# Kernel optimization log

Measured on AMD Instinct MI355X. Metric: run time of the kernel, lower is better.

Reference implementation:

```python
import jax, jax.numpy as jnp
import numpy as np

N_CLASSES = 256
N_AUDIO_CHANS = 1
N_CHANS = 128
N_RES = 128
N_SKIP = 256
N_END = 256
KERNEL = 2
N_LAYERS = 10
N_STACKS = 3
DILATIONS = [2 ** i for _ in range(N_STACKS) for i in range(N_LAYERS)]
L = len(DILATIONS)
DN = ('NCW', 'OIW', 'NCW')


def setup_inputs() -> dict:
    key = jax.random.key(0)
    ks = jax.random.split(key, 16)
    s = 0.05  # small init keeps 30-layer residual stack numerically tame
    inp = {
        'x': jax.random.normal(ks[0], (4, N_AUDIO_CHANS, 16384), jnp.float32),
        'w_shift': jax.random.normal(ks[1], (N_CHANS, N_AUDIO_CHANS, KERNEL), jnp.float32) * s,
        'b_shift': jnp.zeros((N_CHANS,), jnp.float32),
        'conv_w': jax.random.normal(ks[2], (L, 2 * N_RES, N_CHANS, KERNEL), jnp.float32) * s,
        'conv_b': jnp.zeros((L, 2 * N_RES), jnp.float32),
        'res_w': jax.random.normal(ks[3], (L, N_CHANS, N_RES), jnp.float32) * s,
        'res_b': jnp.zeros((L, N_CHANS), jnp.float32),
        'skip_w': jax.random.normal(ks[4], (L, N_SKIP, N_RES), jnp.float32) * s,
        'skip_b': jnp.zeros((L, N_SKIP), jnp.float32),
        'a_w': jax.random.normal(ks[5], (N_END, N_SKIP), jnp.float32) * s,
        'a_b': jnp.zeros((N_END,), jnp.float32),
        'b_w': jax.random.normal(ks[6], (N_CLASSES * N_AUDIO_CHANS, N_END), jnp.float32) * s,
        'b_b': jnp.zeros((N_CLASSES * N_AUDIO_CHANS,), jnp.float32),
    }
    return inp


def _causal_conv(x, w, b, dilation):
    # left-pad by (k-1)*dilation so outputs depend only on past/present
    pad = (w.shape[-1] - 1) * dilation
    xp = jnp.pad(x, ((0, 0), (0, 0), (pad, 0)))
    y = jax.lax.conv_general_dilated(xp, w, window_strides=(1,), padding='VALID',
                                     rhs_dilation=(dilation,), dimension_numbers=DN)
    return y + b[None, :, None]


def reference(x, w_shift, b_shift, conv_w, conv_b, res_w, res_b,
              skip_w, skip_b, a_w, a_b, b_w, b_b):
    N, C, W = x.shape
    # shifted conv: shift input right by one (prepend 0, drop last), then causal conv
    xs = jnp.pad(x, ((0, 0), (0, 0), (1, 0)))[:, :, :-1]
    h = _causal_conv(xs, w_shift, b_shift, 1)  # (N, n_chans, W)

    skips = jnp.zeros((N, N_SKIP, W), h.dtype)
    for l in range(L):
        g = _causal_conv(h, conv_w[l], conv_b[l], DILATIONS[l])  # (N, 2*res, W)
        a, b_gate = jnp.split(g, 2, axis=1)
        gated = a * jax.nn.sigmoid(b_gate)                        # GLU, (N, res, W)
        h = jnp.einsum('or,nrw->now', res_w[l], gated) + res_b[l][None, :, None] + h
        skips = skips + jnp.einsum('or,nrw->now', skip_w[l], gated) + skip_b[l][None, :, None]

    z = jax.nn.relu(skips)
    z = jax.nn.relu(jnp.einsum('os,nsw->now', a_w, z) + a_b[None, :, None])
    logits = jnp.einsum('oe,new->now', b_w, z) + b_b[None, :, None]
    return logits.reshape(N, N_CLASSES, N_AUDIO_CHANS, W)
```

## Files before the change

kernel.cpp:

```cpp
#include <hip/hip_runtime.h>
#include <math.h>


#define NB 4
#define WLEN 16384
#define C 128
#define S 256
#define NLAYERS 30
#define TT 64
#define NTB (WLEN / TT)
#define XROW 264
#define GROW 136

typedef _Float16 half8 __attribute__((ext_vector_type(8)));
typedef _Float16 half4 __attribute__((ext_vector_type(4)));
typedef float floatx4 __attribute__((ext_vector_type(4)));

__device__ __forceinline__ float sigmoidf_(float v) {
    return 1.0f / (1.0f + __expf(-v));
}

__global__ void prep_kernel(const float* __restrict__ conv_w,
                            const float* __restrict__ res_w,
                            const float* __restrict__ skip_w,
                            const float* __restrict__ a_w,
                            const float* __restrict__ b_w,
                            const float* __restrict__ conv_b,
                            const float* __restrict__ skip_b,
                            _Float16* __restrict__ cw,
                            _Float16* __restrict__ rsw,
                            _Float16* __restrict__ skw,
                            _Float16* __restrict__ aw,
                            _Float16* __restrict__ bw,
                            float* __restrict__ cbp,
                            float* __restrict__ ssum) {
    const int ncw = NLAYERS * 256 * 256;
    const int nrs = NLAYERS * 128 * 128;
    const int nsk = NLAYERS * 256 * 128;
    const int nab = 256 * 256;
    const int ncb = NLAYERS * 256;
    const int total = ncw + nrs + nsk + nab + nab + ncb + 256;
    for (int idx = blockIdx.x * blockDim.x + threadIdx.x; idx < total;
         idx += gridDim.x * blockDim.x) {
        int i = idx;
        if (i < ncw) {
            int j = i & 7, lane = (i >> 3) & 63, rest = i >> 9;
            int ks = rest & 7; rest >>= 3;
            int mt = rest & 15; int l = rest >> 4;
            int mp = mt * 16 + (lane & 15);
            int orow = (mp >> 1) + (mp & 1) * 128;
            int k = ks * 32 + (lane >> 4) * 8 + j;
            int tap = k >> 7, c = k & 127;
            cw[i] = (_Float16)conv_w[(((size_t)l * 256 + orow) * 128 + c) * 2 + tap];
        } else if (i < ncw + nrs) {
            i -= ncw;
            int j = i & 7, lane = (i >> 3) & 63, rest = i >> 9;
            int ks = rest & 3; rest >>= 2;
            int mt = rest & 7; int l = rest >> 3;
            int m = mt * 16 + (lane & 15);
            int k = ks * 32 + (lane >> 4) * 8 + j;
            rsw[i] = (_Float16)res_w[((size_t)l * 128 + m) * 128 + k];
        } else if (i < ncw + nrs + nsk) {
            i -= ncw + nrs;
            int j = i & 7, lane = (i >> 3) & 63, rest = i >> 9;
            int ks = rest & 3; rest >>= 2;
            int mt = rest & 15; int l = rest >> 4;
            int m = mt * 16 + (lane & 15);
            int k = ks * 32 + (lane >> 4) * 8 + j;
            skw[i] = (_Float16)skip_w[((size_t)l * 256 + m) * 128 + k];
        } else if (i < ncw + nrs + nsk + nab) {
            i -= ncw + nrs + nsk;
            int j = i & 7, lane = (i >> 3) & 63, rest = i >> 9;
            int ks = rest & 7; int mt = rest >> 3;
            aw[i] = (_Float16)a_w[(mt * 16 + (lane & 15)) * 256 + ks * 32 + (lane >> 4) * 8 + j];
        } else if (i < ncw + nrs + nsk + 2 * nab) {
            i -= ncw + nrs + nsk + nab;
            int j = i & 7, lane = (i >> 3) & 63, rest = i >> 9;
            int ks = rest & 7; int mt = rest >> 3;
            bw[i] = (_Float16)b_w[(mt * 16 + (lane & 15)) * 256 + ks * 32 + (lane >> 4) * 8 + j];
        } else if (i < ncw + nrs + nsk + 2 * nab + ncb) {
            i -= ncw + nrs + nsk + 2 * nab;
            int mp = i & 255; int l = i >> 8;
            cbp[i] = conv_b[l * 256 + (mp >> 1) + (mp & 1) * 128];
        } else {
            i -= ncw + nrs + nsk + 2 * nab + ncb;
            float s = 0.f;
            for (int l = 0; l < NLAYERS; ++l) s += skip_b[l * 256 + i];
            ssum[i] = s;
        }
    }
}

__global__ void front_kernel(const float* __restrict__ x,
                             const float* __restrict__ w_shift,
                             const float* __restrict__ b_shift,
                             _Float16* __restrict__ h) {
    const int n = blockIdx.y;
    const int t = blockIdx.x * 256 + threadIdx.x;
    float x1 = (t >= 1) ? x[n * WLEN + t - 1] : 0.0f;
    float x2 = (t >= 2) ? x[n * WLEN + t - 2] : 0.0f;
    _Float16* hq = h + ((size_t)n * WLEN + t) * 128;
    #pragma unroll
    for (int c0 = 0; c0 < 128; c0 += 8) {
        half8 v;
        #pragma unroll
        for (int j = 0; j < 8; ++j) {
            int c = c0 + j;
            v[j] = (_Float16)fmaf(w_shift[2 * c], x2,
                                  fmaf(w_shift[2 * c + 1], x1, b_shift[c]));
        }
        *(half8*)&hq[c0] = v;
    }
}

template <bool FIRST>
__global__ __launch_bounds__(512, 8) void layer_kernel(
    const _Float16* __restrict__ h_in, _Float16* __restrict__ h_out,
    _Float16* __restrict__ chunk,
    const _Float16* __restrict__ cw, const float* __restrict__ cb,
    const _Float16* __restrict__ rsw, const float* __restrict__ rb,
    const _Float16* __restrict__ skw, const float* __restrict__ ssum, int d) {
    __shared__ _Float16 SMEM[2 * TT * GROW];
    _Float16* X0 = SMEM;
    _Float16* X1 = SMEM + TT * GROW;
    _Float16* G  = X0;
    const int n = blockIdx.y, tb = blockIdx.x, t0 = tb * TT;
    const int tid = threadIdx.x;
    const int wave = __builtin_amdgcn_readfirstlane(tid >> 6);
    const int lane = tid & 63, q = lane >> 4, ml = lane & 15;

    const _Float16* hn = h_in + (size_t)n * WLEN * 128;
    #pragma unroll
    for (int it = 0; it < 4; ++it) {
        int idx = it * 512 + tid;
        int seg = idx & 15;
        int rowc = (idx >> 4) & 63;
        int tap = idx >> 10;
        int src_t = t0 + rowc - (tap ? 0 : d);
        half8 v = (half8)(_Float16)0.0f;
        if (src_t >= 0)
            v = *(const half8*)&hn[(size_t)src_t * 128 + seg * 8];
        _Float16* Xb = tap ? X1 : X0;
        *(half8*)&Xb[rowc * GROW + seg * 8] = v;
    }
    __syncthreads();

    floatx4 acc[2][4];
    #pragma unroll
    for (int mt = 0; mt < 2; ++mt)
        #pragma unroll
        for (int r = 0; r < 4; ++r) {
            float bias = cb[32 * wave + mt * 16 + q * 4 + r];
            #pragma unroll
            for (int nt = 0; nt < 4; ++nt) acc[mt][nt][r] = bias;
        }
    #pragma unroll
    for (int hp = 0; hp < 2; ++hp) {
        const _Float16* Xb = hp ? X1 : X0;
        for (int ks = 0; ks < 4; ++ks) {
            half8 a[2];
            #pragma unroll
            for (int mt = 0; mt < 2; ++mt)
                a[mt] = *(const half8*)&cw[((((2 * wave + mt) * 8) + hp * 4 + ks) * 64 + lane) * 8];
            #pragma unroll
            for (int nt = 0; nt < 4; ++nt) {
                half8 b = *(const half8*)&Xb[(nt * 16 + ml) * GROW + ks * 32 + q * 8];
                #pragma unroll
                for (int mt = 0; mt < 2; ++mt)
                    acc[mt][nt] = __builtin_amdgcn_mfma_f32_16x16x32_f16(a[mt], b, acc[mt][nt], 0, 0, 0);
            }
        }
    }
    __syncthreads();

    #pragma unroll
    for (int mt = 0; mt < 2; ++mt)
        #pragma unroll
        for (int nt = 0; nt < 4; ++nt) {
            float g0 = acc[mt][nt][0] * sigmoidf_(acc[mt][nt][1]);
            float g1 = acc[mt][nt][2] * sigmoidf_(acc[mt][nt][3]);
            _Float16 p[2] = {(_Float16)g0, (_Float16)g1};
            *(uint32_t*)&G[(nt * 16 + ml) * GROW + 16 * wave + mt * 8 + 2 * q] = *(uint32_t*)p;
        }
    __syncthreads();

    {
        floatx4 sacc[2][4];
        #pragma unroll
        for (int mt = 0; mt < 2; ++mt)
            #pragma unroll
            for (int r = 0; r < 4; ++r) {
                float bias = FIRST ? ssum[32 * wave + mt * 16 + q * 4 + r] : 0.0f;
                #pragma unroll
                for (int nt = 0; nt < 4; ++nt) sacc[mt][nt][r] = bias;
            }
        #pragma unroll
        for (int ks = 0; ks < 4; ++ks) {
            half8 a[2];
            #pragma unroll
            for (int mt = 0; mt < 2; ++mt)
                a[mt] = *(const half8*)&skw[((((2 * wave + mt) * 4) + ks) * 64 + lane) * 8];
            #pragma unroll
            for (int nt = 0; nt < 4; ++nt) {
                half8 b = *(const half8*)&G[(nt * 16 + ml) * GROW + ks * 32 + q * 8];
                #pragma unroll
                for (int mt = 0; mt < 2; ++mt)
                    sacc[mt][nt] = __builtin_amdgcn_mfma_f32_16x16x32_f16(a[mt], b, sacc[mt][nt], 0, 0, 0);
            }
        }
        _Float16* cp = chunk + ((size_t)n * NTB + tb) * 16384;
        #pragma unroll
        for (int mt = 0; mt < 2; ++mt)
            #pragma unroll
            for (int nt = 0; nt < 4; ++nt) {
                size_t o = (size_t)((((wave * 2 + mt) * 4) + nt) * 64 + lane) * 4;
                if (FIRST) {
                    half4 v;
                    #pragma unroll
                    for (int r = 0; r < 4; ++r) v[r] = (_Float16)sacc[mt][nt][r];
                    *(half4*)&cp[o] = v;
                } else {
                    half4 v = *(const half4*)&cp[o];
                    half4 w;
                    #pragma unroll
                    for (int r = 0; r < 4; ++r)
                        w[r] = (_Float16)(sacc[mt][nt][r] + (float)v[r]);
                    *(half4*)&cp[o] = w;
                }
            }
    }

    {
        floatx4 racc[4];
        #pragma unroll
        for (int r = 0; r < 4; ++r) {
            float bias = rb[16 * wave + q * 4 + r];
            #pragma unroll
            for (int nt = 0; nt < 4; ++nt) racc[nt][r] = bias;
        }
        #pragma unroll
        for (int ks = 0; ks < 4; ++ks) {
            half8 a = *(const half8*)&rsw[(((wave * 4) + ks) * 64 + lane) * 8];
            #pragma unroll
            for (int nt = 0; nt < 4; ++nt) {
                half8 b = *(const half8*)&G[(nt * 16 + ml) * GROW + ks * 32 + q * 8];
                racc[nt] = __builtin_amdgcn_mfma_f32_16x16x32_f16(a, b, racc[nt], 0, 0, 0);
            }
        }
        _Float16* ho = h_out + (size_t)n * WLEN * 128;
        #pragma unroll
        for (int nt = 0; nt < 4; ++nt) {
            int tt = nt * 16 + ml;
            int c = 16 * wave + q * 4;
            half4 hv = *(const half4*)&X1[tt * GROW + c];
            half4 o;
            #pragma unroll
            for (int r = 0; r < 4; ++r)
                o[r] = (_Float16)(racc[nt][r] + (float)hv[r]);
            *(half4*)&ho[(size_t)(t0 + tt) * 128 + c] = o;
        }
    }
}

__global__ __launch_bounds__(512, 8) void head_kernel(
    float* __restrict__ out, const _Float16* __restrict__ chunk,
    const _Float16* __restrict__ aw, const float* __restrict__ ab,
    const _Float16* __restrict__ bw, const float* __restrict__ bb) {
    __shared__ _Float16 X[TT * XROW];
    const int n = blockIdx.y, tb = blockIdx.x, t0 = tb * TT;
    const int tid = threadIdx.x;
    const int wave = __builtin_amdgcn_readfirstlane(tid >> 6);
    const int lane = tid & 63, q = lane >> 4, ml = lane & 15;

    {
        const _Float16* cp = chunk + ((size_t)n * NTB + tb) * 16384;
        #pragma unroll
        for (int mt = 0; mt < 2; ++mt)
            #pragma unroll
            for (int nt = 0; nt < 4; ++nt) {
                size_t o = (size_t)((((wave * 2 + mt) * 4) + nt) * 64 + lane) * 4;
                half4 v = *(const half4*)&cp[o];
                half4 z;
                #pragma unroll
                for (int r = 0; r < 4; ++r)
                    z[r] = (_Float16)fmaxf((float)v[r], 0.0f);
                *(half4*)&X[(nt * 16 + ml) * XROW + 32 * wave + mt * 16 + q * 4] = z;
            }
    }
    __syncthreads();

    floatx4 acc[2][4];
    #pragma unroll
    for (int mt = 0; mt < 2; ++mt)
        #pragma unroll
        for (int r = 0; r < 4; ++r) {
            float bias = ab[32 * wave + mt * 16 + q * 4 + r];
            #pragma unroll
            for (int nt = 0; nt < 4; ++nt) acc[mt][nt][r] = bias;
        }
    for (int ks = 0; ks < 8; ++ks) {
        half8 a[2];
        #pragma unroll
        for (int mt = 0; mt < 2; ++mt)
            a[mt] = *(const half8*)&aw[((((2 * wave + mt) * 8) + ks) * 64 + lane) * 8];
        #pragma unroll
        for (int nt = 0; nt < 4; ++nt) {
            half8 b = *(const half8*)&X[(nt * 16 + ml) * XROW + ks * 32 + q * 8];
            #pragma unroll
            for (int mt = 0; mt < 2; ++mt)
                acc[mt][nt] = __builtin_amdgcn_mfma_f32_16x16x32_f16(a[mt], b, acc[mt][nt], 0, 0, 0);
        }
    }
    __syncthreads();
    #pragma unroll
    for (int mt = 0; mt < 2; ++mt)
        #pragma unroll
        for (int nt = 0; nt < 4; ++nt) {
            half4 z;
            #pragma unroll
            for (int r = 0; r < 4; ++r)
                z[r] = (_Float16)fmaxf(acc[mt][nt][r], 0.0f);
            *(half4*)&X[(nt * 16 + ml) * XROW + 32 * wave + mt * 16 + q * 4] = z;
        }
    __syncthreads();

    #pragma unroll
    for (int mt = 0; mt < 2; ++mt)
        #pragma unroll
        for (int r = 0; r < 4; ++r) {
            float bias = bb[32 * wave + mt * 16 + q * 4 + r];
            #pragma unroll
            for (int nt = 0; nt < 4; ++nt) acc[mt][nt][r] = bias;
        }
    for (int ks = 0; ks < 8; ++ks) {
        half8 a[2];
        #pragma unroll
        for (int mt = 0; mt < 2; ++mt)
            a[mt] = *(const half8*)&bw[((((2 * wave + mt) * 8) + ks) * 64 + lane) * 8];
        #pragma unroll
        for (int nt = 0; nt < 4; ++nt) {
            half8 b = *(const half8*)&X[(nt * 16 + ml) * XROW + ks * 32 + q * 8];
            #pragma unroll
            for (int mt = 0; mt < 2; ++mt)
                acc[mt][nt] = __builtin_amdgcn_mfma_f32_16x16x32_f16(a[mt], b, acc[mt][nt], 0, 0, 0);
        }
    }
    float* on = out + (size_t)n * S * WLEN;
    #pragma unroll
    for (int mt = 0; mt < 2; ++mt)
        #pragma unroll
        for (int nt = 0; nt < 4; ++nt)
            #pragma unroll
            for (int r = 0; r < 4; ++r) {
                int o = 32 * wave + mt * 16 + q * 4 + r;
                int tt = t0 + nt * 16 + ml;
                on[(size_t)o * WLEN + tt] = acc[mt][nt][r];
            }
}

extern "C" void kernel_launch(void* const* d_in, const int* in_sizes, int n_in,
                              void* d_out, int out_size, void* d_ws, size_t ws_size,
                              hipStream_t stream) {
    (void)in_sizes; (void)n_in; (void)out_size; (void)ws_size;
    const float* x       = (const float*)d_in[0];
    const float* w_shift = (const float*)d_in[1];
    const float* b_shift = (const float*)d_in[2];
    const float* conv_w  = (const float*)d_in[3];
    const float* conv_b  = (const float*)d_in[4];
    const float* res_w   = (const float*)d_in[5];
    const float* res_b   = (const float*)d_in[6];
    const float* skip_w  = (const float*)d_in[7];
    const float* skip_b  = (const float*)d_in[8];
    const float* a_w     = (const float*)d_in[9];
    const float* a_b     = (const float*)d_in[10];
    const float* b_w     = (const float*)d_in[11];
    const float* b_b     = (const float*)d_in[12];
    float* out = (float*)d_out;

    char* ws = (char*)d_ws;
    size_t off = 0;
    _Float16* hA    = (_Float16*)(ws + off); off += (size_t)NB * WLEN * 128 * 2;
    _Float16* hB    = (_Float16*)(ws + off); off += (size_t)NB * WLEN * 128 * 2;
    _Float16* chunk = (_Float16*)(ws + off); off += (size_t)NB * NTB * 16384 * 2;
    _Float16* cw  = (_Float16*)(ws + off); off += (size_t)NLAYERS * 256 * 256 * 2;
    _Float16* rsw = (_Float16*)(ws + off); off += (size_t)NLAYERS * 128 * 128 * 2;
    _Float16* skw = (_Float16*)(ws + off); off += (size_t)NLAYERS * 256 * 128 * 2;
    _Float16* aw  = (_Float16*)(ws + off); off += 256 * 256 * 2;
    _Float16* bw  = (_Float16*)(ws + off); off += 256 * 256 * 2;
    float* cbp  = (float*)(ws + off); off += (size_t)NLAYERS * 256 * 4;
    float* ssum = (float*)(ws + off); off += 256 * 4;

    prep_kernel<<<512, 256, 0, stream>>>(conv_w, res_w, skip_w, a_w, b_w,
                                         conv_b, skip_b,
                                         cw, rsw, skw, aw, bw, cbp, ssum);
    front_kernel<<<dim3(WLEN / 256, NB), 256, 0, stream>>>(x, w_shift, b_shift, hA);

    const dim3 grid(NTB, NB);
    _Float16* hin = hA;
    _Float16* hout = hB;
    for (int l = 0; l < NLAYERS; ++l) {
        int dil = 1 << (l % 10);
        const _Float16* cwp = cw + (size_t)l * 65536;
        const _Float16* rsp = rsw + (size_t)l * 16384;
        const _Float16* skp = skw + (size_t)l * 32768;
        if (l == 0)
            layer_kernel<true><<<grid, 512, 0, stream>>>(
                hin, hout, chunk, cwp, cbp + l * 256,
                rsp, res_b + l * 128, skp, ssum, dil);
        else
            layer_kernel<false><<<grid, 512, 0, stream>>>(
                hin, hout, chunk, cwp, cbp + l * 256,
                rsp, res_b + l * 128, skp, ssum, dil);
        _Float16* tmp = hin; hin = hout; hout = tmp;
    }

    head_kernel<<<grid, 512, 0, stream>>>(out, chunk, aw, a_b, bw, b_b);
}
```

Measured before the change: 1.100 ms.

## Fuse first six dilated layers of each stack into one halo-tiled kernel

Measured after the change: 1.099 ms. No clear change (-0.1%).

```diff
diff --git a/kernel.cpp b/kernel.cpp
--- a/kernel.cpp
+++ b/kernel.cpp
@@ -11,6 +11,7 @@
 #define NTB (WLEN / TT)
 #define XROW 264
 #define GROW 136
+#define HW 128
 
 typedef _Float16 half8 __attribute__((ext_vector_type(8)));
 typedef _Float16 half4 __attribute__((ext_vector_type(4)));
@@ -114,12 +115,189 @@
 }
 
 template <bool FIRST>
+__global__ __launch_bounds__(512, 4) void stack_kernel(
+    const _Float16* __restrict__ h_in, _Float16* __restrict__ h_out,
+    _Float16* __restrict__ chunk,
+    const _Float16* __restrict__ cw0, const float* __restrict__ cb0,
+    const _Float16* __restrict__ rsw0, const float* __restrict__ rb0,
+    const _Float16* __restrict__ skw0, const float* __restrict__ ssum) {
+    __shared__ _Float16 SMEM[2 * HW * GROW];
+    _Float16* H = SMEM;
+    _Float16* G = SMEM + HW * GROW;
+    const int n = blockIdx.y, tb = blockIdx.x, t0 = tb * TT;
+    const int tid = threadIdx.x;
+    const int wave = __builtin_amdgcn_readfirstlane(tid >> 6);
+    const int lane = tid & 63, q = lane >> 4, ml = lane & 15;
+
+    floatx4 sacc[2][4];
+    if (FIRST) {
+        #pragma unroll
+        for (int mt = 0; mt < 2; ++mt)
+            #pragma unroll
+            for (int r = 0; r < 4; ++r) {
+                float bias = ssum[32 * wave + mt * 16 + q * 4 + r];
+                #pragma unroll
+                for (int nt = 0; nt < 4; ++nt) sacc[mt][nt][r] = bias;
+            }
+    } else {
+        const _Float16* cp = chunk + ((size_t)n * NTB + tb) * 16384;
+        #pragma unroll
+        for (int mt = 0; mt < 2; ++mt)
+            #pragma unroll
+            for (int nt = 0; nt < 4; ++nt) {
+                size_t o = (size_t)((((wave * 2 + mt) * 4) + nt) * 64 + lane) * 4;
+                half4 v = *(const half4*)&cp[o];
+                #pragma unroll
+                for (int r = 0; r < 4; ++r) sacc[mt][nt][r] = (float)v[r];
+            }
+    }
+
+    const _Float16* hn = h_in + (size_t)n * WLEN * 128;
+    #pragma unroll
+    for (int it = 0; it < 4; ++it) {
+        int idx = it * 512 + tid;
+        int seg = idx & 15;
+        int w = idx >> 4;
+        int src_t = t0 - 64 + w;
+        half8 v = (half8)(_Float16)0.0f;
+        if (src_t >= 0)
+            v = *(const half8*)&hn[(size_t)src_t * 128 + seg * 8];
+        *(half8*)&H[w * GROW + seg * 8] = v;
+    }
+    __syncthreads();
+
+    const _Float16* cw  = cw0;
+    const float*    cb  = cb0;
+    const _Float16* rsw = rsw0;
+    const float*    rb  = rb0;
+    const _Float16* skw = skw0;
+
+    #pragma clang loop unroll(disable)
+    for (int j = 0; j < 6; ++j) {
+        const int d = 1 << j;
+
+        #pragma unroll
+        for (int np = 0; np < 2; ++np) {
+            floatx4 acc[2][4];
+            #pragma unroll
+            for (int mt = 0; mt < 2; ++mt)
+                #pragma unroll
+                for (int r = 0; r < 4; ++r) {
+                    float bias = cb[32 * wave + mt * 16 + q * 4 + r];
+                    #pragma unroll
+                    for (int nt = 0; nt < 4; ++nt) acc[mt][nt][r] = bias;
+                }
+            #pragma unroll
+            for (int hp = 0; hp < 2; ++hp) {
+                for (int ks = 0; ks < 4; ++ks) {
+                    half8 a[2];
+                    #pragma unroll
+                    for (int mt = 0; mt < 2; ++mt)
+                        a[mt] = *(const half8*)&cw[((((2 * wave + mt) * 8) + hp * 4 + ks) * 64 + lane) * 8];
+                    #pragma unroll
+                    for (int nt = 0; nt < 4; ++nt) {
+                        int row = np * 64 + nt * 16 + ml;
+                        if (!hp) { row -= d; if (row < 0) row = 0; }
+                        half8 b = *(const half8*)&H[row * GROW + ks * 32 + q * 8];
+                        #pragma unroll
+                        for (int mt = 0; mt < 2; ++mt)
+                            acc[mt][nt] = __builtin_amdgcn_mfma_f32_16x16x32_f16(a[mt], b, acc[mt][nt], 0, 0, 0);
+                    }
+                }
+            }
+            #pragma unroll
+            for (int mt = 0; mt < 2; ++mt)
+                #pragma unroll
+                for (int nt = 0; nt < 4; ++nt) {
+                    float g0 = acc[mt][nt][0] * sigmoidf_(acc[mt][nt][1]);
+                    float g1 = acc[mt][nt][2] * sigmoidf_(acc[mt][nt][3]);
+                    _Float16 p[2] = {(_Float16)g0, (_Float16)g1};
+                    *(uint32_t*)&G[(np * 64 + nt * 16 + ml) * GROW + 16 * wave + mt * 8 + 2 * q] = *(uint32_t*)p;
+                }
+        }
+        __syncthreads();
+
+        #pragma unroll
+        for (int ks = 0; ks < 4; ++ks) {
+            half8 a[2];
+            #pragma unroll
+            for (int mt = 0; mt < 2; ++mt)
+                a[mt] = *(const half8*)&skw[((((2 * wave + mt) * 4) + ks) * 64 + lane) * 8];
+            #pragma unroll
+            for (int nt = 0; nt < 4; ++nt) {
+                half8 b = *(const half8*)&G[(64 + nt * 16 + ml) * GROW + ks * 32 + q * 8];
+                #pragma unroll
+                for (int mt = 0; mt < 2; ++mt)
+                    sacc[mt][nt] = __builtin_amdgcn_mfma_f32_16x16x32_f16(a[mt], b, sacc[mt][nt], 0, 0, 0);
+            }
+        }
+
+        #pragma unroll
+        for (int np = 0; np < 2; ++np) {
+            floatx4 racc[4];
+            #pragma unroll
+            for (int r = 0; r < 4; ++r) {
+                float bias = rb[16 * wave + q * 4 + r];
+                #pragma unroll
+                for (int nt = 0; nt < 4; ++nt) racc[nt][r] = bias;
+            }
+            #pragma unroll
+            for (int ks = 0; ks < 4; ++ks) {
+                half8 a = *(const half8*)&rsw[(((wave * 4) + ks) * 64 + lane) * 8];
+                #pragma unroll
+                for (int nt = 0; nt < 4; ++nt) {
+                    half8 b = *(const half8*)&G[(np * 64 + nt * 16 + ml) * GROW + ks * 32 + q * 8];
+                    racc[nt] = __builtin_amdgcn_mfma_f32_16x16x32_f16(a, b, racc[nt], 0, 0, 0);
+                }
+            }
+            #pragma unroll
+            for (int nt = 0; nt < 4; ++nt) {
+                int w = np * 64 + nt * 16 + ml;
+                int c = 16 * wave + q * 4;
+                half4 hv = *(const half4*)&H[w * GROW + c];
+                half4 o;
+                #pragma unroll
+                for (int r = 0; r < 4; ++r)
+                    o[r] = (_Float16)(racc[nt][r] + (float)hv[r]);
+                *(half4*)&H[w * GROW + c] = o;
+            }
+        }
+        __syncthreads();
+
+        cw  += 65536; cb += 256; rsw += 16384; rb += 128; skw += 32768;
+    }
+
+    _Float16* ho = h_out + (size_t)n * WLEN * 128;
+    #pragma unroll
+    for (int it = 0; it < 2; ++it) {
+        int idx = it * 512 + tid;
+        int seg = idx & 15;
+        int w64 = idx >> 4;
+        *(half8*)&ho[(size_t)(t0 + w64) * 128 + seg * 8] =
+            *(const half8*)&H[(64 + w64) * GROW + seg * 8];
+    }
+
+    {
+        _Float16* cp = chunk + ((size_t)n * NTB + tb) * 16384;
+        #pragma unroll
+        for (int mt = 0; mt < 2; ++mt)
+            #pragma unroll
+            for (int nt = 0; nt < 4; ++nt) {
+                size_t o = (size_t)((((wave * 2 + mt) * 4) + nt) * 64 + lane) * 4;
+                half4 v;
+                #pragma unroll
+                for (int r = 0; r < 4; ++r) v[r] = (_Float16)sacc[mt][nt][r];
+                *(half4*)&cp[o] = v;
+            }
+    }
+}
+
 __global__ __launch_bounds__(512, 8) void layer_kernel(
     const _Float16* __restrict__ h_in, _Float16* __restrict__ h_out,
     _Float16* __restrict__ chunk,
     const _Float16* __restrict__ cw, const float* __restrict__ cb,
     const _Float16* __restrict__ rsw, const float* __restrict__ rb,
-    const _Float16* __restrict__ skw, const float* __restrict__ ssum, int d) {
+    const _Float16* __restrict__ skw, int d) {
     __shared__ _Float16 SMEM[2 * TT * GROW];
     _Float16* X0 = SMEM;
     _Float16* X1 = SMEM + TT * GROW;
@@ -189,11 +367,9 @@
         #pragma unroll
         for (int mt = 0; mt < 2; ++mt)
             #pragma unroll
-            for (int r = 0; r < 4; ++r) {
-                float bias = FIRST ? ssum[32 * wave + mt * 16 + q * 4 + r] : 0.0f;
-                #pragma unroll
-                for (int nt = 0; nt < 4; ++nt) sacc[mt][nt][r] = bias;
-            }
+            for (int nt = 0; nt < 4; ++nt)
+                #pragma unroll
+                for (int r = 0; r < 4; ++r) sacc[mt][nt][r] = 0.0f;
         #pragma unroll
         for (int ks = 0; ks < 4; ++ks) {
             half8 a[2];
@@ -214,19 +390,12 @@
             #pragma unroll
             for (int nt = 0; nt < 4; ++nt) {
                 size_t o = (size_t)((((wave * 2 + mt) * 4) + nt) * 64 + lane) * 4;
-                if (FIRST) {
-                    half4 v;
-                    #pragma unroll
-                    for (int r = 0; r < 4; ++r) v[r] = (_Float16)sacc[mt][nt][r];
-                    *(half4*)&cp[o] = v;
-                } else {
-                    half4 v = *(const half4*)&cp[o];
-                    half4 w;
-                    #pragma unroll
-                    for (int r = 0; r < 4; ++r)
-                        w[r] = (_Float16)(sacc[mt][nt][r] + (float)v[r]);
-                    *(half4*)&cp[o] = w;
-                }
+                half4 v = *(const half4*)&cp[o];
+                half4 w;
+                #pragma unroll
+                for (int r = 0; r < 4; ++r)
+                    w[r] = (_Float16)(sacc[mt][nt][r] + (float)v[r]);
+                *(half4*)&cp[o] = w;
             }
     }
 
@@ -398,20 +567,31 @@
     const dim3 grid(NTB, NB);
     _Float16* hin = hA;
     _Float16* hout = hB;
-    for (int l = 0; l < NLAYERS; ++l) {
-        int dil = 1 << (l % 10);
-        const _Float16* cwp = cw + (size_t)l * 65536;
-        const _Float16* rsp = rsw + (size_t)l * 16384;
-        const _Float16* skp = skw + (size_t)l * 32768;
-        if (l == 0)
-            layer_kernel<true><<<grid, 512, 0, stream>>>(
-                hin, hout, chunk, cwp, cbp + l * 256,
-                rsp, res_b + l * 128, skp, ssum, dil);
+    for (int s = 0; s < 3; ++s) {
+        const int l0 = s * 10;
+        if (s == 0)
+            stack_kernel<true><<<grid, 512, 0, stream>>>(
+                hin, hout, chunk,
+                cw + (size_t)l0 * 65536, cbp + l0 * 256,
+                rsw + (size_t)l0 * 16384, res_b + l0 * 128,
+                skw + (size_t)l0 * 32768, ssum);
         else
-            layer_kernel<false><<<grid, 512, 0, stream>>>(
-                hin, hout, chunk, cwp, cbp + l * 256,
-                rsp, res_b + l * 128, skp, ssum, dil);
-        _Float16* tmp = hin; hin = hout; hout = tmp;
+            stack_kernel<false><<<grid, 512, 0, stream>>>(
+                hin, hout, chunk,
+                cw + (size_t)l0 * 65536, cbp + l0 * 256,
+                rsw + (size_t)l0 * 16384, res_b + l0 * 128,
+                skw + (size_t)l0 * 32768, ssum);
+        { _Float16* tmp = hin; hin = hout; hout = tmp; }
+        for (int jj = 6; jj < 10; ++jj) {
+            const int l = l0 + jj;
+            const int dil = 1 << jj;
+            layer_kernel<<<grid, 512, 0, stream>>>(
+                hin, hout, chunk,
+                cw + (size_t)l * 65536, cbp + l * 256,
+                rsw + (size_t)l * 16384, res_b + l * 128,
+                skw + (size_t)l * 32768, dil);
+            _Float16* tmp = hin; hin = hout; hout = tmp;
+        }
     }
 
     head_kernel<<<grid, 512, 0, stream>>>(out, chunk, aw, a_b, bw, b_b);
```
